# Kernel optimization log

Hardware: AMD Instinct MI355X
Metric: run time of the kernel (lower is better)

Reference implementation:

```python
import jax, jax.numpy as jnp
import numpy as np

H = 32        # hiddenSize
OUT = 256     # output_size
T = 60        # num_frames
EPS = 1e-5


def setup_inputs() -> dict:
    key = jax.random.key(0)
    ks = jax.random.split(key, 16)
    s = 0.05
    rn = lambda k, shp: (jax.random.normal(k, shp, dtype=jnp.float32) * s)
    return {
        "x": jax.random.normal(ks[0], (1, T, 63), dtype=jnp.float32),
        "w00": rn(ks[1], (63, 63)), "b00": rn(ks[2], (63,)),
        "w01": rn(ks[3], (64, 63)), "b01": rn(ks[4], (64,)),
        "ln_g": jnp.ones((64,), jnp.float32), "ln_b": jnp.zeros((64,), jnp.float32),
        "w_ih": rn(ks[5], (4 * H, 64)), "w_hh": rn(ks[6], (4 * H, H)),
        "b_ih": rn(ks[7], (4 * H,)), "b_hh": rn(ks[8], (4 * H,)),
        "bn_g": jnp.ones((H,), jnp.float32), "bn_b": jnp.zeros((H,), jnp.float32),
        "w10": rn(ks[9], (32, H)), "b10": rn(ks[10], (32,)),
        "w11": rn(ks[11], (32, 32)), "b11": rn(ks[12], (32,)),
        "w12": rn(ks[13], (OUT, 32)), "b12": rn(ks[14], (OUT,)),
    }


def _forward(x, w00, b00, w01, b01, ln_g, ln_b, w_ih, w_hh, b_ih, b_hh,
             bn_g, bn_b, w10, b10, w11, b11, w12, b12):
    # x: [1, T, 63] -> scan over T frames (fused MLP + LayerNorm + LSTM cell)
    xs = jnp.transpose(x, (1, 0, 2))  # [T, 1, 63]

    def step(carry, xt):  # xt: [1, 63]
        h, c = carry
        f = jax.nn.relu(xt @ w00.T + b00)          # [1, 63]
        f = jax.nn.relu(f @ w01.T + b01)           # [1, 64]
        mu = jnp.mean(f, axis=-1, keepdims=True)
        var = jnp.mean((f - mu) ** 2, axis=-1, keepdims=True)
        f = (f - mu) * jax.lax.rsqrt(var + EPS) * ln_g + ln_b
        gates = f @ w_ih.T + b_ih + h @ w_hh.T + b_hh  # [1, 4H]
        i_g, f_g, g_g, o_g = jnp.split(gates, 4, axis=-1)
        c = jax.nn.sigmoid(f_g) * c + jax.nn.sigmoid(i_g) * jnp.tanh(g_g)
        h = jax.nn.sigmoid(o_g) * jnp.tanh(c)
        return (h, c), None

    h0 = jnp.zeros((1, H), x.dtype)
    c0 = jnp.zeros((1, H), x.dtype)
    (h, _), _ = jax.lax.scan(step, (h0, c0), xs)
    # BatchNorm1d in eval mode (running_mean=0, running_var=1)
    out = h * jax.lax.rsqrt(jnp.float32(1.0) + EPS) * bn_g + bn_b
    out = jax.nn.relu(out @ w10.T + b10)
    out = jax.nn.relu(out @ w11.T + b11)
    return out @ w12.T + b12  # [1, OUT]


def reference(x, w00, b00, w01, b01, ln_g, ln_b, w_ih, w_hh, b_ih, b_hh,
              bn_g, bn_b, w10, b10, w11, b11, w12, b12):
    return _forward(x, w00, b00, w01, b01, ln_g, ln_b, w_ih, w_hh, b_ih, b_hh,
                    bn_g, bn_b, w10, b10, w11, b11, w12, b12)
```

## Files before the change

kernel.cpp:

```cpp
#include <hip/hip_runtime.h>

#define EPS 1e-5f

__device__ __forceinline__ float fsigm(float x) { return 1.0f / (1.0f + __expf(-x)); }
__device__ __forceinline__ float ftanh(float x) {
    float e = __expf(-2.0f * x);
    return (1.0f - e) / (1.0f + e);
}
__device__ __forceinline__ float rdl(float v, int k) {
    return __int_as_float(__builtin_amdgcn_readlane(__float_as_int(v), k));
}

__device__ __forceinline__ void warm_loop(int iters, float* sink) {
    float s = (float)(blockIdx.x * 64 + threadIdx.x) * 1e-6f + 0.5f;
    float a0 = s, a1 = s + 0.1f, a2 = s + 0.2f, a3 = s + 0.3f;
    float a4 = s + 0.4f, a5 = s + 0.5f, a6 = s + 0.6f, a7 = s + 0.7f;
    for (int i = 0; i < iters; i++) {
        a0 = fmaf(a0, 0.9999999f, 1e-7f);
        a1 = fmaf(a1, 0.9999999f, 1e-7f);
        a2 = fmaf(a2, 0.9999999f, 1e-7f);
        a3 = fmaf(a3, 0.9999999f, 1e-7f);
        a4 = fmaf(a4, 0.9999999f, 1e-7f);
        a5 = fmaf(a5, 0.9999999f, 1e-7f);
        a6 = fmaf(a6, 0.9999999f, 1e-7f);
        a7 = fmaf(a7, 0.9999999f, 1e-7f);
    }
    sink[threadIdx.x] = ((a0 + a1) + (a2 + a3)) + ((a4 + a5) + (a6 + a7));
}

__global__ __launch_bounds__(64) void frontend_kernel(
    const float* __restrict__ x,
    const float* __restrict__ w00, const float* __restrict__ b00,
    const float* __restrict__ w01, const float* __restrict__ b01,
    const float* __restrict__ ln_g, const float* __restrict__ ln_b,
    const float* __restrict__ w_ih,
    const float* __restrict__ b_ih, const float* __restrict__ b_hh,
    float* __restrict__ Gx, float* __restrict__ warm_sink)
{
    __shared__ float smem[16324];
    const int j = threadIdx.x;
    const int t = blockIdx.x;

    if (t >= 60) {
        warm_loop(250, warm_sink + blockIdx.x * 64);
        return;
    }

    float* w00s = smem;
    float* w01s = smem + 3972;
    float* wihT = smem + 8004;
    float* scr  = smem + 16196;

    {
        const float4* g4 = (const float4*)w00;
        float4* s4 = (float4*)w00s;
        for (int i = j; i < 992; i += 64) s4[i] = g4[i];
        if (j == 0) w00s[3968] = w00[3968];
    }
    {
        const float4* g4 = (const float4*)w01;
        float4* s4 = (float4*)w01s;
        for (int i = j; i < 1008; i += 64) s4[i] = g4[i];
    }
    for (int r = j; r < 128; r += 64) {
        const float4* row = (const float4*)(w_ih + r * 64);
        #pragma unroll
        for (int q = 0; q < 16; q++) {
            float4 v = row[q];
            wihT[(4 * q + 0) * 128 + r] = v.x;
            wihT[(4 * q + 1) * 128 + r] = v.y;
            wihT[(4 * q + 2) * 128 + r] = v.z;
            wihT[(4 * q + 3) * 128 + r] = v.w;
        }
    }
    scr[j] = (j < 63) ? x[t * 63 + j] : 0.0f;
    __syncthreads();

    float f0 = 0.0f;
    if (j < 63) {
        float acc = b00[j];
        const float* wr = w00s + j * 63;
        #pragma unroll
        for (int k = 0; k < 63; k++) acc += scr[k] * wr[k];
        f0 = fmaxf(acc, 0.0f);
    }
    __syncthreads();
    scr[j] = f0;
    __syncthreads();

    float acc = b01[j];
    {
        const float* wr = w01s + j * 63;
        #pragma unroll
        for (int k = 0; k < 63; k++) acc += scr[k] * wr[k];
    }
    float f1 = fmaxf(acc, 0.0f);

    float s = f1, sq = f1 * f1;
    #pragma unroll
    for (int off = 32; off > 0; off >>= 1) {
        s  += __shfl_xor(s, off);
        sq += __shfl_xor(sq, off);
    }
    float mu  = s * (1.0f / 64.0f);
    float var = sq * (1.0f / 64.0f) - mu * mu;
    float f   = (f1 - mu) * rsqrtf(var + EPS) * ln_g[j] + ln_b[j];
    __syncthreads();
    scr[64 + j] = f;
    __syncthreads();

    float a0 = b_ih[j] + b_hh[j];
    float a1 = b_ih[j + 64] + b_hh[j + 64];
    #pragma unroll
    for (int k = 0; k < 64; k++) {
        float fk = scr[64 + k];
        a0 += fk * wihT[k * 128 + j];
        a1 += fk * wihT[k * 128 + 64 + j];
    }
    Gx[t * 128 + j]      = a0;
    Gx[t * 128 + 64 + j] = a1;
}

__global__ __launch_bounds__(64) void scan_kernel(
    const float* __restrict__ Gx,
    const float* __restrict__ w_hh,
    const float* __restrict__ bn_g, const float* __restrict__ bn_b,
    const float* __restrict__ w10, const float* __restrict__ b10,
    const float* __restrict__ w11, const float* __restrict__ b11,
    const float* __restrict__ w12, const float* __restrict__ b12,
    float* __restrict__ out, float* __restrict__ warm_sink)
{
    __shared__ float gxs[7808];
    const int j = threadIdx.x;

    if (blockIdx.x != 0) {
        warm_loop(1750, warm_sink + blockIdx.x * 64);
        return;
    }

    float wA[32], wB[32];
    {
        const float4* r0 = (const float4*)(w_hh + j * 32);
        const float4* r1 = (const float4*)(w_hh + (j + 64) * 32);
        #pragma unroll
        for (int q = 0; q < 8; q++) {
            float4 a = r0[q];
            float4 b = r1[q];
            wA[4 * q] = a.x; wA[4 * q + 1] = a.y; wA[4 * q + 2] = a.z; wA[4 * q + 3] = a.w;
            wB[4 * q] = b.x; wB[4 * q + 1] = b.y; wB[4 * q + 2] = b.z; wB[4 * q + 3] = b.w;
        }
    }
    {
        const float4* g4 = (const float4*)Gx;
        float4* s4 = (float4*)gxs;
        for (int i = j; i < 1920; i += 64) s4[i] = g4[i];
        gxs[7680 + j] = 0.0f;
        gxs[7744 + j] = 0.0f;
    }
    __syncthreads();

    float c = 0.0f, hn = 0.0f;
    float gA = gxs[j], gB = gxs[64 + j];
    for (int t = 0; t < 60; t++) {
        float a0a = gA, a0b = 0.f, a0c = 0.f, a0d = 0.f;
        float a1a = gB, a1b = 0.f, a1c = 0.f, a1d = 0.f;
        gA = gxs[(t + 1) * 128 + j];
        gB = gxs[(t + 1) * 128 + 64 + j];
        #pragma unroll
        for (int k = 0; k < 8; k++) {
            float h0 = rdl(hn, k);
            float h1 = rdl(hn, k + 8);
            float h2 = rdl(hn, k + 16);
            float h3 = rdl(hn, k + 24);
            a0a += h0 * wA[k];      a1a += h0 * wB[k];
            a0b += h1 * wA[k + 8];  a1b += h1 * wB[k + 8];
            a0c += h2 * wA[k + 16]; a1c += h2 * wB[k + 16];
            a0d += h3 * wA[k + 24]; a1d += h3 * wB[k + 24];
        }
        float a0 = (a0a + a0b) + (a0c + a0d);
        float a1 = (a1a + a1b) + (a1c + a1d);
        float fv = __shfl_xor(a0, 32);
        float ov = __shfl_xor(a1, 32);
        float ig = fsigm(a0) * ftanh(a1);
        c  = fsigm(fv) * c + ig;
        hn = fsigm(ov) * ftanh(c);
    }

    const float rs = rsqrtf(1.0f + EPS);
    const int ro = j & 31;
    float acc = b10[ro];
    #pragma unroll
    for (int k = 0; k < 32; k++) {
        float hk = rdl(hn, k);
        float hb = hk * rs * bn_g[k] + bn_b[k];
        acc += w10[ro * 32 + k] * hb;
    }
    float o1 = fmaxf(acc, 0.0f);

    acc = b11[ro];
    #pragma unroll
    for (int k = 0; k < 32; k++) acc += w11[ro * 32 + k] * rdl(o1, k);
    float o2 = fmaxf(acc, 0.0f);

    float a[4];
    #pragma unroll
    for (int r = 0; r < 4; r++) a[r] = b12[j + 64 * r];
    #pragma unroll
    for (int k = 0; k < 32; k++) {
        float h2 = rdl(o2, k);
        #pragma unroll
        for (int r = 0; r < 4; r++) a[r] += w12[(j + 64 * r) * 32 + k] * h2;
    }
    #pragma unroll
    for (int r = 0; r < 4; r++) out[j + 64 * r] = a[r];
}

extern "C" void kernel_launch(void* const* d_in, const int* in_sizes, int n_in,
                              void* d_out, int out_size, void* d_ws, size_t ws_size,
                              hipStream_t stream) {
    const float* x    = (const float*)d_in[0];
    const float* w00  = (const float*)d_in[1];
    const float* b00  = (const float*)d_in[2];
    const float* w01  = (const float*)d_in[3];
    const float* b01  = (const float*)d_in[4];
    const float* ln_g = (const float*)d_in[5];
    const float* ln_b = (const float*)d_in[6];
    const float* w_ih = (const float*)d_in[7];
    const float* w_hh = (const float*)d_in[8];
    const float* b_ih = (const float*)d_in[9];
    const float* b_hh = (const float*)d_in[10];
    const float* bn_g = (const float*)d_in[11];
    const float* bn_b = (const float*)d_in[12];
    const float* w10  = (const float*)d_in[13];
    const float* b10  = (const float*)d_in[14];
    const float* w11  = (const float*)d_in[15];
    const float* b11  = (const float*)d_in[16];
    const float* w12  = (const float*)d_in[17];
    const float* b12  = (const float*)d_in[18];
    float* out = (float*)d_out;
    float* Gx        = (float*)d_ws;
    float* warm_sink = (float*)((char*)d_ws + 65536);

    frontend_kernel<<<256, 64, 0, stream>>>(x, w00, b00, w01, b01, ln_g, ln_b,
                                            w_ih, b_ih, b_hh, Gx, warm_sink);
    scan_kernel<<<256, 64, 0, stream>>>(Gx, w_hh, bn_g, bn_b, w10, b10,
                                        w11, b11, w12, b12, out, warm_sink);
}
```

Measured before the change: 135.0 us.

## Drop GPU warm-up blocks, use hardware reciprocal, pack recurrent weights as float2

New measurement: 127.5 us. 1.06x faster.

```diff
diff --git a/kernel.cpp b/kernel.cpp
--- a/kernel.cpp
+++ b/kernel.cpp
@@ -2,30 +2,14 @@
 
 #define EPS 1e-5f
 
-__device__ __forceinline__ float fsigm(float x) { return 1.0f / (1.0f + __expf(-x)); }
+__device__ __forceinline__ float frcp(float x) { return __builtin_amdgcn_rcpf(x); }
+__device__ __forceinline__ float fsigm(float x) { return frcp(1.0f + __expf(-x)); }
 __device__ __forceinline__ float ftanh(float x) {
     float e = __expf(-2.0f * x);
-    return (1.0f - e) / (1.0f + e);
+    return (1.0f - e) * frcp(1.0f + e);
 }
 __device__ __forceinline__ float rdl(float v, int k) {
     return __int_as_float(__builtin_amdgcn_readlane(__float_as_int(v), k));
-}
-
-__device__ __forceinline__ void warm_loop(int iters, float* sink) {
-    float s = (float)(blockIdx.x * 64 + threadIdx.x) * 1e-6f + 0.5f;
-    float a0 = s, a1 = s + 0.1f, a2 = s + 0.2f, a3 = s + 0.3f;
-    float a4 = s + 0.4f, a5 = s + 0.5f, a6 = s + 0.6f, a7 = s + 0.7f;
-    for (int i = 0; i < iters; i++) {
-        a0 = fmaf(a0, 0.9999999f, 1e-7f);
-        a1 = fmaf(a1, 0.9999999f, 1e-7f);
-        a2 = fmaf(a2, 0.9999999f, 1e-7f);
-        a3 = fmaf(a3, 0.9999999f, 1e-7f);
-        a4 = fmaf(a4, 0.9999999f, 1e-7f);
-        a5 = fmaf(a5, 0.9999999f, 1e-7f);
-        a6 = fmaf(a6, 0.9999999f, 1e-7f);
-        a7 = fmaf(a7, 0.9999999f, 1e-7f);
-    }
-    sink[threadIdx.x] = ((a0 + a1) + (a2 + a3)) + ((a4 + a5) + (a6 + a7));
 }
 
 __global__ __launch_bounds__(64) void frontend_kernel(
@@ -35,21 +19,16 @@
     const float* __restrict__ ln_g, const float* __restrict__ ln_b,
     const float* __restrict__ w_ih,
     const float* __restrict__ b_ih, const float* __restrict__ b_hh,
-    float* __restrict__ Gx, float* __restrict__ warm_sink)
+    float* __restrict__ Gx)
 {
     __shared__ float smem[16324];
-    const int j = threadIdx.x;
-    const int t = blockIdx.x;
-
-    if (t >= 60) {
-        warm_loop(250, warm_sink + blockIdx.x * 64);
-        return;
-    }
-
     float* w00s = smem;
     float* w01s = smem + 3972;
     float* wihT = smem + 8004;
     float* scr  = smem + 16196;
+
+    const int j = threadIdx.x;
+    const int t = blockIdx.x;
 
     {
         const float4* g4 = (const float4*)w00;
@@ -128,17 +107,12 @@
     const float* __restrict__ w10, const float* __restrict__ b10,
     const float* __restrict__ w11, const float* __restrict__ b11,
     const float* __restrict__ w12, const float* __restrict__ b12,
-    float* __restrict__ out, float* __restrict__ warm_sink)
+    float* __restrict__ out)
 {
     __shared__ float gxs[7808];
     const int j = threadIdx.x;
 
-    if (blockIdx.x != 0) {
-        warm_loop(1750, warm_sink + blockIdx.x * 64);
-        return;
-    }
-
-    float wA[32], wB[32];
+    float2 wAB[32];
     {
         const float4* r0 = (const float4*)(w_hh + j * 32);
         const float4* r1 = (const float4*)(w_hh + (j + 64) * 32);
@@ -146,8 +120,10 @@
         for (int q = 0; q < 8; q++) {
             float4 a = r0[q];
             float4 b = r1[q];
-            wA[4 * q] = a.x; wA[4 * q + 1] = a.y; wA[4 * q + 2] = a.z; wA[4 * q + 3] = a.w;
-            wB[4 * q] = b.x; wB[4 * q + 1] = b.y; wB[4 * q + 2] = b.z; wB[4 * q + 3] = b.w;
+            wAB[4 * q + 0] = make_float2(a.x, b.x);
+            wAB[4 * q + 1] = make_float2(a.y, b.y);
+            wAB[4 * q + 2] = make_float2(a.z, b.z);
+            wAB[4 * q + 3] = make_float2(a.w, b.w);
         }
     }
     {
@@ -162,8 +138,10 @@
     float c = 0.0f, hn = 0.0f;
     float gA = gxs[j], gB = gxs[64 + j];
     for (int t = 0; t < 60; t++) {
-        float a0a = gA, a0b = 0.f, a0c = 0.f, a0d = 0.f;
-        float a1a = gB, a1b = 0.f, a1c = 0.f, a1d = 0.f;
+        float2 acc0 = make_float2(gA, gB);
+        float2 acc1 = make_float2(0.f, 0.f);
+        float2 acc2 = make_float2(0.f, 0.f);
+        float2 acc3 = make_float2(0.f, 0.f);
         gA = gxs[(t + 1) * 128 + j];
         gB = gxs[(t + 1) * 128 + 64 + j];
         #pragma unroll
@@ -172,13 +150,13 @@
             float h1 = rdl(hn, k + 8);
             float h2 = rdl(hn, k + 16);
             float h3 = rdl(hn, k + 24);
-            a0a += h0 * wA[k];      a1a += h0 * wB[k];
-            a0b += h1 * wA[k + 8];  a1b += h1 * wB[k + 8];
-            a0c += h2 * wA[k + 16]; a1c += h2 * wB[k + 16];
-            a0d += h3 * wA[k + 24]; a1d += h3 * wB[k + 24];
+            acc0.x += h0 * wAB[k].x;      acc0.y += h0 * wAB[k].y;
+            acc1.x += h1 * wAB[k + 8].x;  acc1.y += h1 * wAB[k + 8].y;
+            acc2.x += h2 * wAB[k + 16].x; acc2.y += h2 * wAB[k + 16].y;
+            acc3.x += h3 * wAB[k + 24].x; acc3.y += h3 * wAB[k + 24].y;
         }
-        float a0 = (a0a + a0b) + (a0c + a0d);
-        float a1 = (a1a + a1b) + (a1c + a1d);
+        float a0 = (acc0.x + acc1.x) + (acc2.x + acc3.x);
+        float a1 = (acc0.y + acc1.y) + (acc2.y + acc3.y);
         float fv = __shfl_xor(a0, 32);
         float ov = __shfl_xor(a1, 32);
         float ig = fsigm(a0) * ftanh(a1);
@@ -238,11 +216,10 @@
     const float* w12  = (const float*)d_in[17];
     const float* b12  = (const float*)d_in[18];
     float* out = (float*)d_out;
-    float* Gx        = (float*)d_ws;
-    float* warm_sink = (float*)((char*)d_ws + 65536);
-
-    frontend_kernel<<<256, 64, 0, stream>>>(x, w00, b00, w01, b01, ln_g, ln_b,
-                                            w_ih, b_ih, b_hh, Gx, warm_sink);
-    scan_kernel<<<256, 64, 0, stream>>>(Gx, w_hh, bn_g, bn_b, w10, b10,
-                                        w11, b11, w12, b12, out, warm_sink);
-}
+    float* Gx  = (float*)d_ws;
+
+    frontend_kernel<<<60, 64, 0, stream>>>(x, w00, b00, w01, b01, ln_g, ln_b,
+                                           w_ih, b_ih, b_hh, Gx);
+    scan_kernel<<<1, 64, 0, stream>>>(Gx, w_hh, bn_g, bn_b, w10, b10,
+                                      w11, b11, w12, b12, out);
+}
```
